# Kernel optimization log

Hardware: AMD Instinct MI355X
Metric: run time of the kernel (lower is better)

Reference implementation:

```python
import jax, jax.numpy as jnp
import numpy as np

N_NODES = 50000
N_EDGES = 600000
N_GRAPHS = 256
BN_EPS = 1e-5
NEG_SLOPE = 0.2  # PyG GATv2 default leaky_relu slope


def segment_softmax(logits, seg, num_segments):
    # logits: [E, H], softmax over edges sharing the same destination node
    m = jax.ops.segment_max(logits, seg, num_segments=num_segments)
    e = jnp.exp(logits - m[seg])
    s = jax.ops.segment_sum(e, seg, num_segments=num_segments)
    return e / (s[seg] + 1e-16)


def gatv2_layer(h, edge_attr, src, dst, Wl, bl, Wr, br, We, att, bias, concat):
    # PyG GATv2Conv (share_weights=False, edge_dim set), eval mode (no dropout)
    heads, out_c = att.shape
    N = h.shape[0]
    xl = (h @ Wl + bl).reshape(N, heads, out_c)  # messages from source
    xr = (h @ Wr + br).reshape(N, heads, out_c)  # destination term
    em = (edge_attr @ We).reshape(-1, heads, out_c)
    z = jax.nn.leaky_relu(xl[src] + xr[dst] + em, NEG_SLOPE)  # [E,H,C]
    logits = jnp.einsum('ehc,hc->eh', z, att)
    alpha = segment_softmax(logits, dst, N)  # [E,H]
    out = jax.ops.segment_sum(xl[src] * alpha[:, :, None], dst, num_segments=N)
    out = out.reshape(N, heads * out_c) if concat else out.mean(axis=1)
    return out + bias


def batch_norm(h, gamma, beta):
    mu = h.mean(axis=0)
    var = h.var(axis=0)
    return gamma * (h - mu) * jax.lax.rsqrt(var + BN_EPS) + beta


def setup_inputs() -> dict:
    key = jax.random.key(0)
    ks = jax.random.split(key, 32)
    F, Fe, H, C = 64, 16, 4, 64
    HC = H * C

    def w(k, shape):
        return jax.random.normal(k, shape, dtype=jnp.float32) * 0.1

    inp = {
        'x': jax.random.normal(ks[0], (N_NODES, F), dtype=jnp.float32),
        'edge_attr': jax.random.normal(ks[1], (N_EDGES, Fe), dtype=jnp.float32),
        'edge_index': jax.random.randint(ks[2], (2, N_EDGES), 0, N_NODES, dtype=jnp.int32),
        'batch': jnp.sort(jax.random.randint(ks[3], (N_NODES,), 0, N_GRAPHS, dtype=jnp.int32)),
        # input projection
        'W_in': w(ks[4], (F, C)), 'b_in': jnp.zeros((C,), jnp.float32),
        'Wl0': w(ks[5], (C, HC)), 'bl0': jnp.zeros((HC,), jnp.float32),
        'Wr0': w(ks[6], (C, HC)), 'br0': jnp.zeros((HC,), jnp.float32),
        'We0': w(ks[7], (Fe, HC)),
        'att0': w(ks[8], (H, C)), 'bias0': jnp.zeros((HC,), jnp.float32),
        'g0': jnp.ones((HC,), jnp.float32), 'beta0': jnp.zeros((HC,), jnp.float32),
        'Wl1': w(ks[9], (HC, HC)), 'bl1': jnp.zeros((HC,), jnp.float32),
        'Wr1': w(ks[10], (HC, HC)), 'br1': jnp.zeros((HC,), jnp.float32),
        'We1': w(ks[11], (Fe, HC)),
        'att1': w(ks[12], (H, C)), 'bias1': jnp.zeros((C,), jnp.float32),
        'g1': jnp.ones((C,), jnp.float32), 'beta1': jnp.zeros((C,), jnp.float32),
        # MLP head 64 -> 32 -> 16 -> 1
        'Wm1': w(ks[13], (C, C // 2)), 'bm1': jnp.zeros((C // 2,), jnp.float32),
        'Wm2': w(ks[14], (C // 2, C // 4)), 'bm2': jnp.zeros((C // 4,), jnp.float32),
        'Wm3': w(ks[15], (C // 4, 1)), 'bm3': jnp.zeros((1,), jnp.float32),
    }
    return inp


def reference(x, edge_attr, W_in, b_in,
              Wl0, bl0, Wr0, br0, We0, att0, bias0, g0, beta0,
              Wl1, bl1, Wr1, br1, We1, att1, bias1, g1, beta1,
              Wm1, bm1, Wm2, bm2, Wm3, bm3,
              edge_index, batch):
    src, dst = edge_index[0], edge_index[1]
    h = jax.nn.relu(x @ W_in + b_in)
    h = gatv2_layer(h, edge_attr, src, dst, Wl0, bl0, Wr0, br0, We0, att0, bias0, True)
    h = batch_norm(h, g0, beta0)
    h = jax.nn.relu(h)  # dropout is identity in eval mode
    h = gatv2_layer(h, edge_attr, src, dst, Wl1, bl1, Wr1, br1, We1, att1, bias1, False)
    h = batch_norm(h, g1, beta1)
    # global mean pool over graphs
    cnt = jax.ops.segment_sum(jnp.ones((h.shape[0],), h.dtype), batch, num_segments=N_GRAPHS)
    pooled = jax.ops.segment_sum(h, batch, num_segments=N_GRAPHS) / jnp.maximum(cnt, 1.0)[:, None]
    z = jax.nn.relu(pooled @ Wm1 + bm1)
    z = jax.nn.relu(z @ Wm2 + bm2)
    return z @ Wm3 + bm3  # [N_GRAPHS, 1]
```

## Files before the change

### kernel.cpp

```cpp
#include <hip/hip_runtime.h>
#include <math.h>

constexpr int NN = 50000;
constexpr int NE = 600000;
constexpr int NG = 256;
constexpr int SB = (NN + 255) / 256;
constexpr float kBnEps = 1e-5f;
constexpr float kSlope = 0.2f;

typedef _Float16 f16x8 __attribute__((ext_vector_type(8)));
typedef float f32x16 __attribute__((ext_vector_type(16)));

__device__ __forceinline__ float rdlane(float v, int l) {
    return __builtin_bit_cast(float, __builtin_amdgcn_readlane(__builtin_bit_cast(int, v), l));
}

template <int CTRL>
__device__ __forceinline__ float dppadd(float v) {
    int t = __builtin_amdgcn_mov_dpp(__builtin_bit_cast(int, v), CTRL, 0xF, 0xF, true);
    return v + __builtin_bit_cast(float, t);
}
__device__ __forceinline__ float sum16(float v) {
    v = dppadd<0xB1>(v);
    v = dppadd<0x4E>(v);
    v = dppadd<0x141>(v);
    v = dppadd<0x140>(v);
    return v;
}

__device__ __forceinline__ float4 fma4(float a, float4 b, float4 c) {
    c.x = fmaf(a, b.x, c.x); c.y = fmaf(a, b.y, c.y);
    c.z = fmaf(a, b.z, c.z); c.w = fmaf(a, b.w, c.w);
    return c;
}

__global__ __launch_bounds__(256) void k_hist(const int* __restrict__ dst, int* __restrict__ cnt)
{
    int e = blockIdx.x * 256 + threadIdx.x;
    if (e < NE) atomicAdd(&cnt[dst[e]], 1);
}

__global__ __launch_bounds__(256) void k_scanA(const int* __restrict__ cnt,
                                               int* __restrict__ offs, int* __restrict__ bsum)
{
    __shared__ int s[256];
    int tid = threadIdx.x;
    int i = blockIdx.x * 256 + tid;
    int v = (i < NN) ? cnt[i] : 0;
    s[tid] = v;
    __syncthreads();
    #pragma unroll
    for (int d = 1; d < 256; d <<= 1) {
        int u = (tid >= d) ? s[tid - d] : 0;
        __syncthreads();
        s[tid] += u;
        __syncthreads();
    }
    if (i < NN) offs[i] = s[tid];
    if (tid == 255) bsum[blockIdx.x] = s[255];
}

__global__ __launch_bounds__(256) void k_scanC(const int* __restrict__ cnt,
                                               const int* __restrict__ bsum,
                                               int* __restrict__ offs, int* __restrict__ cur)
{
    __shared__ int sred[256];
    int t = threadIdx.x;
    int b = blockIdx.x;
    int v = (t < SB && t < b) ? bsum[t] : 0;
    sred[t] = v;
    __syncthreads();
    #pragma unroll
    for (int d = 128; d > 0; d >>= 1) {
        if (t < d) sred[t] += sred[t + d];
        __syncthreads();
    }
    int pre = sred[0];
    int i = b * 256 + t;
    if (i > NN) return;
    if (i == NN) { offs[NN] = NE; return; }
    int w = offs[i] - cnt[i] + pre;
    offs[i] = w;
    cur[i] = w;
}

__global__ __launch_bounds__(256) void k_scatter_light(const int* __restrict__ dst,
                                                       const int* __restrict__ src,
                                                       int* __restrict__ cur,
                                                       int2* __restrict__ se)
{
    int e = blockIdx.x * 256 + threadIdx.x;
    if (e < NE) {
        int p = atomicAdd(&cur[dst[e]], 1);
        se[p] = make_int2(src[e], e);
    }
}

__device__ __forceinline__ void prep_w_body(int T, const float* __restrict__ WL,
                                            const float* __restrict__ WR,
                                            _Float16* __restrict__ bhi,
                                            _Float16* __restrict__ blo)
{
    int g   = T & 1;
    int col = (T >> 1) & 511;
    int kt  = T >> 10;
    const float* W = (col < 256) ? WL : WR;
    int c = col & 255;
    f16x8 h8, l8;
    #pragma unroll
    for (int i = 0; i < 8; ++i) {
        float v = W[(size_t)(kt * 16 + g * 8 + i) * 256 + c];
        _Float16 hv = (_Float16)v;
        h8[i] = hv;
        l8[i] = (_Float16)(v - (float)hv);
    }
    *(f16x8*)(bhi + (size_t)T * 8) = h8;
    *(f16x8*)(blo + (size_t)T * 8) = l8;
}

__global__ __launch_bounds__(256) void k_prep_all(
    const float* __restrict__ Wl0, const float* __restrict__ Wr0,
    _Float16* __restrict__ bhi0, _Float16* __restrict__ blo0,
    const float* __restrict__ Wl1, const float* __restrict__ Wr1,
    _Float16* __restrict__ bhi1, _Float16* __restrict__ blo1)
{
    if (blockIdx.x < 16) {
        int T = blockIdx.x * 256 + threadIdx.x;
        prep_w_body(T, Wl0, Wr0, bhi0, blo0);
    } else {
        int T = (blockIdx.x - 16) * 256 + threadIdx.x;
        prep_w_body(T, Wl1, Wr1, bhi1, blo1);
    }
}

__global__ __launch_bounds__(512) void k_lin0_mfma(
    const float* __restrict__ x, const float* __restrict__ Win,
    const float* __restrict__ bin,
    const _Float16* __restrict__ Bhi, const _Float16* __restrict__ Blo,
    const float* __restrict__ bl, const float* __restrict__ br,
    float* __restrict__ outl, float* __restrict__ outr)
{
    __shared__ float h0s[64][68];
    __shared__ f16x8 Apack[2][4][128];
    int tid = threadIdx.x;
    int lane = tid & 63, wave = tid >> 6;
    int row0 = blockIdx.x * 64;

    {
        int rbase = row0 + wave * 8;
        float xreg[8];
        #pragma unroll
        for (int j = 0; j < 8; ++j) {
            int row = rbase + j; if (row >= NN) row = NN - 1;
            xreg[j] = x[(size_t)row * 64 + lane];
        }
        float b0 = bin[lane];
        float h0r[8];
        #pragma unroll
        for (int j = 0; j < 8; ++j) h0r[j] = b0;
        for (int k = 0; k < 64; ++k) {
            float w = Win[k * 64 + lane];
            #pragma unroll
            for (int j = 0; j < 8; ++j) h0r[j] = fmaf(rdlane(xreg[j], k), w, h0r[j]);
        }
        #pragma unroll
        for (int j = 0; j < 8; ++j)
            h0s[wave * 8 + j][lane] = fmaxf(h0r[j], 0.f);
    }
    __syncthreads();

    {
        int row = tid >> 3;
        int o = (tid & 7) * 8;
        f16x8 hi8, lo8;
        #pragma unroll
        for (int i = 0; i < 8; ++i) {
            float v = h0s[row][o + i];
            _Float16 hv = (_Float16)v;
            hi8[i] = hv;
            lo8[i] = (_Float16)(v - (float)hv);
        }
        int kt = o >> 4, g2 = (o >> 3) & 1;
        int slot = (g2 * 64 + row) ^ kt;
        Apack[0][kt][slot] = hi8;
        Apack[1][kt][slot] = lo8;
    }
    __syncthreads();

    int g = lane >> 5;
    int rowtile = wave >> 2;
    int colbase = (wave & 3) * 128 + (lane & 31);
    int aslot = g * 64 + rowtile * 32 + (lane & 31);
    f32x16 acc[4];
    #pragma unroll
    for (int nt = 0; nt < 4; ++nt)
        #pragma unroll
        for (int r = 0; r < 16; ++r) acc[nt][r] = 0.f;

    const f16x8* bh = (const f16x8*)Bhi;
    const f16x8* bo = (const f16x8*)Blo;
    size_t fbase = (size_t)colbase * 2 + g;

    #pragma unroll 1
    for (int kt = 0; kt < 4; ++kt) {
        f16x8 ahi = Apack[0][kt][aslot ^ kt];
        f16x8 alo = Apack[1][kt][aslot ^ kt];
        f16x8 wh[4], wl[4];
        #pragma unroll
        for (int nt = 0; nt < 4; ++nt) {
            size_t fi = fbase + (size_t)kt * 1024 + nt * 64;
            wh[nt] = bh[fi];
            wl[nt] = bo[fi];
        }
        #pragma unroll
        for (int nt = 0; nt < 4; ++nt)
            acc[nt] = __builtin_amdgcn_mfma_f32_32x32x16_f16(ahi, wh[nt], acc[nt], 0, 0, 0);
        #pragma unroll
        for (int nt = 0; nt < 4; ++nt)
            acc[nt] = __builtin_amdgcn_mfma_f32_32x32x16_f16(alo, wh[nt], acc[nt], 0, 0, 0);
        #pragma unroll
        for (int nt = 0; nt < 4; ++nt)
            acc[nt] = __builtin_amdgcn_mfma_f32_32x32x16_f16(ahi, wl[nt], acc[nt], 0, 0, 0);
    }

    #pragma unroll
    for (int nt = 0; nt < 4; ++nt) {
        int col = colbase + nt * 32;
        bool isR = col >= 256;
        int c = isR ? col - 256 : col;
        float bv = isR ? br[c] : bl[c];
        float* outp = isR ? outr : outl;
        #pragma unroll
        for (int r = 0; r < 16; ++r) {
            int rowoff = (r & 3) + 8 * (r >> 2) + 4 * g;
            int grow = row0 + rowtile * 32 + rowoff;
            if (grow < NN)
                outp[(size_t)grow * 256 + c] = acc[nt][r] + bv;
        }
    }
}

__global__ __launch_bounds__(512) void k_linear2_mfma(
    const float* __restrict__ h, const _Float16* __restrict__ Bhi,
    const _Float16* __restrict__ Blo, const float* __restrict__ bl,
    const float* __restrict__ br, const float* __restrict__ scale,
    const float* __restrict__ shift, float* __restrict__ outl,
    float* __restrict__ outr)
{
    __shared__ f16x8 Apack[2][16][128];
    int tid = threadIdx.x;
    int lane = tid & 63, wave = tid >> 6;
    int row0 = blockIdx.x * 64;

    {
        int row  = tid >> 3;
        int koff = (tid & 7) * 32;
        int grow = row0 + row; if (grow >= NN) grow = NN - 1;
        const float* hp = h + (size_t)grow * 256 + koff;
        #pragma unroll
        for (int j2 = 0; j2 < 4; ++j2) {
            int o = koff + j2 * 8;
            float4 a  = *(const float4*)(hp + j2 * 8);
            float4 b  = *(const float4*)(hp + j2 * 8 + 4);
            float4 s0 = *(const float4*)(scale + o);
            float4 s1 = *(const float4*)(scale + o + 4);
            float4 f0 = *(const float4*)(shift + o);
            float4 f1 = *(const float4*)(shift + o + 4);
            float va[8] = {
                fmaxf(fmaf(a.x, s0.x, f0.x), 0.f), fmaxf(fmaf(a.y, s0.y, f0.y), 0.f),
                fmaxf(fmaf(a.z, s0.z, f0.z), 0.f), fmaxf(fmaf(a.w, s0.w, f0.w), 0.f),
                fmaxf(fmaf(b.x, s1.x, f1.x), 0.f), fmaxf(fmaf(b.y, s1.y, f1.y), 0.f),
                fmaxf(fmaf(b.z, s1.z, f1.z), 0.f), fmaxf(fmaf(b.w, s1.w, f1.w), 0.f)};
            f16x8 hi8, lo8;
            #pragma unroll
            for (int i = 0; i < 8; ++i) {
                _Float16 hv = (_Float16)va[i];
                hi8[i] = hv;
                lo8[i] = (_Float16)(va[i] - (float)hv);
            }
            int kt = o >> 4, g = (o >> 3) & 1;
            int slot = (g * 64 + row) ^ (kt & 7);
            Apack[0][kt][slot] = hi8;
            Apack[1][kt][slot] = lo8;
        }
    }
    __syncthreads();

    int g = lane >> 5;
    int rowtile = wave >> 2;
    int colbase = (wave & 3) * 128 + (lane & 31);
    int aslot = g * 64 + rowtile * 32 + (lane & 31);
    f32x16 acc[4];
    #pragma unroll
    for (int nt = 0; nt < 4; ++nt)
        #pragma unroll
        for (int r = 0; r < 16; ++r) acc[nt][r] = 0.f;

    const f16x8* bh = (const f16x8*)Bhi;
    const f16x8* bo = (const f16x8*)Blo;
    size_t fbase = (size_t)colbase * 2 + g;

    #pragma unroll 1
    for (int kt = 0; kt < 16; ++kt) {
        f16x8 ahi = Apack[0][kt][aslot ^ (kt & 7)];
        f16x8 alo = Apack[1][kt][aslot ^ (kt & 7)];
        f16x8 wh[4], wl[4];
        #pragma unroll
        for (int nt = 0; nt < 4; ++nt) {
            size_t fi = fbase + (size_t)kt * 1024 + nt * 64;
            wh[nt] = bh[fi];
            wl[nt] = bo[fi];
        }
        #pragma unroll
        for (int nt = 0; nt < 4; ++nt)
            acc[nt] = __builtin_amdgcn_mfma_f32_32x32x16_f16(ahi, wh[nt], acc[nt], 0, 0, 0);
        #pragma unroll
        for (int nt = 0; nt < 4; ++nt)
            acc[nt] = __builtin_amdgcn_mfma_f32_32x32x16_f16(alo, wh[nt], acc[nt], 0, 0, 0);
        #pragma unroll
        for (int nt = 0; nt < 4; ++nt)
            acc[nt] = __builtin_amdgcn_mfma_f32_32x32x16_f16(ahi, wl[nt], acc[nt], 0, 0, 0);
    }

    #pragma unroll
    for (int nt = 0; nt < 4; ++nt) {
        int col = colbase + nt * 32;
        bool isR = col >= 256;
        int c = isR ? col - 256 : col;
        float bv = isR ? br[c] : bl[c];
        float* outp = isR ? outr : outl;
        #pragma unroll
        for (int r = 0; r < 16; ++r) {
            int rowoff = (r & 3) + 8 * (r >> 2) + 4 * g;
            int grow = row0 + rowtile * 32 + rowoff;
            if (grow < NN)
                outp[(size_t)grow * 256 + c] = acc[nt][r] + bv;
        }
    }
}

template <bool CONCAT, int NPW>
__global__ __launch_bounds__(256) void k_attn(
    const float* __restrict__ xl, const float* __restrict__ xr,
    const int2* __restrict__ se, const float* __restrict__ ea,
    const float* __restrict__ We, const float* __restrict__ att,
    const int* __restrict__ offs, const float* __restrict__ bias,
    float* __restrict__ out)
{
    int tid = threadIdx.x;
    int lane = tid & 63, wave = tid >> 6;
    float4 wr[16];
    #pragma unroll
    for (int k = 0; k < 16; ++k) wr[k] = ((const float4*)(We + k * 256))[lane];
    float4 ar = ((const float4*)att)[lane];

    int g16 = lane >> 4;
    int k16 = lane & 15;
    int nodebase = (blockIdx.x * 4 + wave) * NPW;
    if (nodebase >= NN) return;

    for (int nn = 0; nn < NPW; ++nn) {
        int n = nodebase + nn;
        if (n >= NN) break;
        int beg = offs[n], end = offs[n + 1];
        float4 xr4 = ((const float4*)(xr + (size_t)n * 256))[lane];

        float m = -INFINITY, ssum = 0.f;
        float4 acc = make_float4(0.f, 0.f, 0.f, 0.f);

        float nea = 0.f;
        float4 nx0, nx1, nx2, nx3;

        auto loadbatch = [&](int i) {
            int idx = i + g16;
            if (idx > end - 1) idx = end - 1;
            int2 sv2 = se[idx];
            nea = ea[(size_t)sv2.y * 16 + k16];
            int sv = sv2.x;
            int s0 = __builtin_amdgcn_readlane(sv, 0);
            int s1 = __builtin_amdgcn_readlane(sv, 16);
            int s2 = __builtin_amdgcn_readlane(sv, 32);
            int s3 = __builtin_amdgcn_readlane(sv, 48);
            nx0 = ((const float4*)(xl + (size_t)s0 * 256))[lane];
            nx1 = ((const float4*)(xl + (size_t)s1 * 256))[lane];
            nx2 = ((const float4*)(xl + (size_t)s2 * 256))[lane];
            nx3 = ((const float4*)(xl + (size_t)s3 * 256))[lane];
        };

        if (beg < end) loadbatch(beg);

        for (int i = beg; i < end; i += 4) {
            float cea = nea;
            float4 x0 = nx0, x1 = nx1, x2 = nx2, x3 = nx3;
            if (i + 4 < end) loadbatch(i + 4);

            float p[4];
            #pragma unroll
            for (int g = 0; g < 4; ++g) {
                float4 xg = (g == 0) ? x0 : (g == 1) ? x1 : (g == 2) ? x2 : x3;
                float4 em = xr4;
                #pragma unroll
                for (int k = 0; k < 16; ++k) {
                    float a = rdlane(cea, g * 16 + k);
                    em.x = fmaf(a, wr[k].x, em.x);
                    em.y = fmaf(a, wr[k].y, em.y);
                    em.z = fmaf(a, wr[k].z, em.z);
                    em.w = fmaf(a, wr[k].w, em.w);
                }
                float z0 = xg.x + em.x;
                float z1 = xg.y + em.y;
                float z2 = xg.z + em.z;
                float z3 = xg.w + em.w;
                z0 = (z0 > 0.f) ? z0 : kSlope * z0;
                z1 = (z1 > 0.f) ? z1 : kSlope * z1;
                z2 = (z2 > 0.f) ? z2 : kSlope * z2;
                z3 = (z3 > 0.f) ? z3 : kSlope * z3;
                float pv = fmaf(z0, ar.x, fmaf(z1, ar.y, fmaf(z2, ar.z, z3 * ar.w)));
                pv = sum16(pv);
                p[g] = (i + g < end) ? pv : -INFINITY;
            }
            float pm = fmaxf(fmaxf(p[0], p[1]), fmaxf(p[2], p[3]));
            float mn = fmaxf(m, pm);
            float sc = __expf(m - mn);
            float w0 = __expf(p[0] - mn);
            float w1 = __expf(p[1] - mn);
            float w2 = __expf(p[2] - mn);
            float w3 = __expf(p[3] - mn);
            ssum = fmaf(ssum, sc, (w0 + w1) + (w2 + w3));
            acc.x = fmaf(acc.x, sc, fmaf(w0, x0.x, fmaf(w1, x1.x, fmaf(w2, x2.x, w3 * x3.x))));
            acc.y = fmaf(acc.y, sc, fmaf(w0, x0.y, fmaf(w1, x1.y, fmaf(w2, x2.y, w3 * x3.y))));
            acc.z = fmaf(acc.z, sc, fmaf(w0, x0.z, fmaf(w1, x1.z, fmaf(w2, x2.z, w3 * x3.z))));
            acc.w = fmaf(acc.w, sc, fmaf(w0, x0.w, fmaf(w1, x1.w, fmaf(w2, x2.w, w3 * x3.w))));
            m = mn;
        }

        float inv = 1.f / (ssum + 1e-16f);
        if (CONCAT) {
            float4 b4 = ((const float4*)bias)[lane];
            float4 o;
            o.x = fmaf(acc.x, inv, b4.x);
            o.y = fmaf(acc.y, inv, b4.y);
            o.z = fmaf(acc.z, inv, b4.z);
            o.w = fmaf(acc.w, inv, b4.w);
            ((float4*)(out + (size_t)n * 256))[lane] = o;
        } else {
            float v0 = acc.x * inv, v1 = acc.y * inv, v2 = acc.z * inv, v3 = acc.w * inv;
            v0 += __shfl_xor(v0, 16, 64); v0 += __shfl_xor(v0, 32, 64);
            v1 += __shfl_xor(v1, 16, 64); v1 += __shfl_xor(v1, 32, 64);
            v2 += __shfl_xor(v2, 16, 64); v2 += __shfl_xor(v2, 32, 64);
            v3 += __shfl_xor(v3, 16, 64); v3 += __shfl_xor(v3, 32, 64);
            if (lane < 16) {
                float4 b4 = ((const float4*)bias)[lane];
                float4 o;
                o.x = fmaf(0.25f, v0, b4.x);
                o.y = fmaf(0.25f, v1, b4.y);
                o.z = fmaf(0.25f, v2, b4.z);
                o.w = fmaf(0.25f, v3, b4.w);
                ((float4*)(out + (size_t)n * 64))[lane] = o;
            }
        }
    }
}

template <int CH>
__global__ __launch_bounds__(256) void k_bn_stats(const float* __restrict__ h,
                                                  float* __restrict__ sum,
                                                  float* __restrict__ sumsq)
{
    constexpr int RP = 256 / CH;
    int tid = threadIdx.x;
    int c = tid % CH;
    int rsub = tid / CH;
    float s = 0.f, q = 0.f;
    #pragma unroll 4
    for (int n = blockIdx.x * RP + rsub; n < NN; n += gridDim.x * RP) {
        float v = h[(size_t)n * CH + c];
        s += v; q = fmaf(v, v, q);
    }
    __shared__ float ls[256], lq[256];
    ls[tid] = s; lq[tid] = q;
    __syncthreads();
    if (tid < CH) {
        #pragma unroll
        for (int r = 1; r < RP; ++r) { s += ls[tid + r * CH]; q += lq[tid + r * CH]; }
        atomicAdd(&sum[tid], s);
        atomicAdd(&sumsq[tid], q);
    }
}

__global__ void k_bn_finalize(const float* __restrict__ sum, const float* __restrict__ sumsq,
                              const float* __restrict__ g, const float* __restrict__ beta,
                              float* __restrict__ scale, float* __restrict__ shift, int CH)
{
    int c = threadIdx.x;
    if (c >= CH) return;
    float inv_n = 1.f / (float)NN;
    float mu = sum[c] * inv_n;
    float var = sumsq[c] * inv_n - mu * mu;
    float sc = g[c] / sqrtf(var + kBnEps);
    scale[c] = sc;
    shift[c] = fmaf(-mu, sc, beta[c]);
}

__global__ __launch_bounds__(256) void k_pool_mlp(
    const float* __restrict__ h2, const float* __restrict__ bns,
    const float* __restrict__ bnq, const float* __restrict__ gam,
    const float* __restrict__ beta, const int* __restrict__ batch,
    const float* __restrict__ Wm1, const float* __restrict__ bm1,
    const float* __restrict__ Wm2, const float* __restrict__ bm2,
    const float* __restrict__ Wm3, const float* __restrict__ bm3,
    float* __restrict__ out)
{
    int g = blockIdx.x, tid = threadIdx.x;
    int lane = tid & 63, wave = tid >> 6;
    __shared__ int sb[2];
    if (tid < 2) {
        int target = g + tid;
        int lo = 0, hi = NN;
        while (lo < hi) {
            int mid = (lo + hi) >> 1;
            if (batch[mid] < target) lo = mid + 1; else hi = mid;
        }
        sb[tid] = lo;
    }
    __syncthreads();
    int s = sb[0], e = sb[1];
    float inv_n = 1.f / (float)NN;
    float mu = bns[lane] * inv_n;
    float var = bnq[lane] * inv_n - mu * mu;
    float sc = gam[lane] / sqrtf(var + kBnEps);
    float sh = fmaf(-mu, sc, beta[lane]);
    float acc = 0.f;
    #pragma unroll 4
    for (int n = s + wave; n < e; n += 4)
        acc += fmaf(h2[(size_t)n * 64 + lane], sc, sh);
    __shared__ float red[4][64];
    red[wave][lane] = acc;
    __syncthreads();
    __shared__ float p[64], z1[32], z2[16];
    if (tid < 64) {
        float cnt = (float)(e - s);
        float a = red[0][tid] + red[1][tid] + red[2][tid] + red[3][tid];
        p[tid] = a / fmaxf(cnt, 1.f);
    }
    __syncthreads();
    if (tid < 32) {
        float a = bm1[tid];
        #pragma unroll
        for (int k = 0; k < 64; ++k) a = fmaf(p[k], Wm1[k * 32 + tid], a);
        z1[tid] = fmaxf(a, 0.f);
    }
    __syncthreads();
    if (tid < 16) {
        float a = bm2[tid];
        #pragma unroll
        for (int k = 0; k < 32; ++k) a = fmaf(z1[k], Wm2[k * 16 + tid], a);
        z2[tid] = fmaxf(a, 0.f);
    }
    __syncthreads();
    if (tid == 0) {
        float a = bm3[0];
        #pragma unroll
        for (int k = 0; k < 16; ++k) a = fmaf(z2[k], Wm3[k], a);
        out[g] = a;
    }
}

extern "C" void kernel_launch(void* const* d_in, const int* in_sizes, int n_in,
                              void* d_out, int out_size, void* d_ws, size_t ws_size,
                              hipStream_t stream)
{
    const float* x     = (const float*)d_in[0];
    const float* ea    = (const float*)d_in[1];
    const int*   ei    = (const int*)d_in[2];
    const int*   bat   = (const int*)d_in[3];
    const float* W_in  = (const float*)d_in[4];
    const float* b_in  = (const float*)d_in[5];
    const float* Wl0   = (const float*)d_in[6];
    const float* bl0   = (const float*)d_in[7];
    const float* Wr0   = (const float*)d_in[8];
    const float* br0   = (const float*)d_in[9];
    const float* We0   = (const float*)d_in[10];
    const float* att0  = (const float*)d_in[11];
    const float* bias0 = (const float*)d_in[12];
    const float* g0    = (const float*)d_in[13];
    const float* beta0 = (const float*)d_in[14];
    const float* Wl1   = (const float*)d_in[15];
    const float* bl1   = (const float*)d_in[16];
    const float* Wr1   = (const float*)d_in[17];
    const float* br1   = (const float*)d_in[18];
    const float* We1   = (const float*)d_in[19];
    const float* att1  = (const float*)d_in[20];
    const float* bias1 = (const float*)d_in[21];
    const float* g1    = (const float*)d_in[22];
    const float* beta1 = (const float*)d_in[23];
    const float* Wm1   = (const float*)d_in[24];
    const float* bm1   = (const float*)d_in[25];
    const float* Wm2   = (const float*)d_in[26];
    const float* bm2   = (const float*)d_in[27];
    const float* Wm3   = (const float*)d_in[28];
    const float* bm3   = (const float*)d_in[29];
    const int* src = ei;
    const int* dst = ei + NE;
    float* out = (float*)d_out;

    char* p = (char*)d_ws;
    auto take = [&](size_t nbytes) -> char* {
        char* q = p;
        p += (nbytes + 255) & ~(size_t)255;
        return q;
    };
    char* z0 = p;
    int*   hist   = (int*)take((size_t)NN * 4);
    float* bns0   = (float*)take(256 * 4);
    float* bnq0   = (float*)take(256 * 4);
    float* bns1   = (float*)take(64 * 4);
    float* bnq1   = (float*)take(64 * 4);
    size_t zbytes = (size_t)(p - z0);
    int*   offs   = (int*)take((size_t)(NN + 1) * 4);
    int*   curs   = (int*)take((size_t)NN * 4);
    int*   bsum   = (int*)take((size_t)SB * 4);
    int2*  se     = (int2*)take((size_t)NE * 8);
    float* h2     = (float*)take((size_t)NN * 64 * 4);
    float* xl     = (float*)take((size_t)NN * 256 * 4);
    float* xr     = (float*)take((size_t)NN * 256 * 4);
    float* h1     = (float*)take((size_t)NN * 256 * 4);
    float* scale0 = (float*)take(256 * 4);
    float* shift0 = (float*)take(256 * 4);
    _Float16* Bhi1 = (_Float16*)take((size_t)256 * 512 * 2);
    _Float16* Blo1 = (_Float16*)take((size_t)256 * 512 * 2);
    _Float16* Bhi0 = (_Float16*)take((size_t)64 * 512 * 2);
    _Float16* Blo0 = (_Float16*)take((size_t)64 * 512 * 2);

    hipMemsetAsync(z0, 0, zbytes, stream);

    k_hist<<<(NE + 255) / 256, 256, 0, stream>>>(dst, hist);
    k_prep_all<<<80, 256, 0, stream>>>(Wl0, Wr0, Bhi0, Blo0, Wl1, Wr1, Bhi1, Blo1);
    k_scanA<<<SB, 256, 0, stream>>>(hist, offs, bsum);
    k_scanC<<<SB, 256, 0, stream>>>(hist, bsum, offs, curs);
    k_scatter_light<<<(NE + 255) / 256, 256, 0, stream>>>(dst, src, curs, se);

    constexpr int NPW = 2;
    int attn_blocks = (NN + 4 * NPW - 1) / (4 * NPW);
    int lin_blocks = (NN + 63) / 64;

    k_lin0_mfma<<<lin_blocks, 512, 0, stream>>>(
        x, W_in, b_in, Bhi0, Blo0, bl0, br0, xl, xr);
    k_attn<true, NPW><<<attn_blocks, 256, 0, stream>>>(
        xl, xr, se, ea, We0, att0, offs, bias0, h1);
    k_bn_stats<256><<<256, 256, 0, stream>>>(h1, bns0, bnq0);
    k_bn_finalize<<<1, 256, 0, stream>>>(bns0, bnq0, g0, beta0, scale0, shift0, 256);

    k_linear2_mfma<<<lin_blocks, 512, 0, stream>>>(
        h1, Bhi1, Blo1, bl1, br1, scale0, shift0, xl, xr);
    k_attn<false, NPW><<<attn_blocks, 256, 0, stream>>>(
        xl, xr, se, ea, We1, att1, offs, bias1, h2);
    k_bn_stats<64><<<256, 256, 0, stream>>>(h2, bns1, bnq1);

    k_pool_mlp<<<NG, 256, 0, stream>>>(h2, bns1, bnq1, g1, beta1, bat,
                                       Wm1, bm1, Wm2, bm2, Wm3, bm3, out);
}
```

Before: 706.2 us.

## Make layer-1 linear persistent with weights held in registers

The layer-1 linear kernel becomes persistent with a fixed grid of 512 blocks. Each block owns one 128-column quarter of the output, and each wave keeps its 32-column slice of the split-f16 weights in registers for the whole kernel. Blocks loop over 32-row tiles, staging BN+ReLU-transformed activations into LDS, so weights are no longer reloaded from global memory for every 64-row tile. In exchange, each activation row is now read by four blocks and every tile needs two barriers. The BN-stats kernels are also launched with four times as many blocks.

```diff
diff --git a/kernel.cpp b/kernel.cpp
--- a/kernel.cpp
+++ b/kernel.cpp
@@ -240,101 +240,93 @@
     }
 }
 
-__global__ __launch_bounds__(512) void k_linear2_mfma(
+__global__ __launch_bounds__(256) void k_linear2_mfma(
     const float* __restrict__ h, const _Float16* __restrict__ Bhi,
     const _Float16* __restrict__ Blo, const float* __restrict__ bl,
     const float* __restrict__ br, const float* __restrict__ scale,
     const float* __restrict__ shift, float* __restrict__ outl,
     float* __restrict__ outr)
 {
-    __shared__ f16x8 Apack[2][16][128];
+    __shared__ f16x8 Apack[2][16][64];
     int tid = threadIdx.x;
     int lane = tid & 63, wave = tid >> 6;
-    int row0 = blockIdx.x * 64;
-
-    {
-        int row  = tid >> 3;
-        int koff = (tid & 7) * 32;
-        int grow = row0 + row; if (grow >= NN) grow = NN - 1;
-        const float* hp = h + (size_t)grow * 256 + koff;
-        #pragma unroll
-        for (int j2 = 0; j2 < 4; ++j2) {
-            int o = koff + j2 * 8;
-            float4 a  = *(const float4*)(hp + j2 * 8);
-            float4 b  = *(const float4*)(hp + j2 * 8 + 4);
-            float4 s0 = *(const float4*)(scale + o);
-            float4 s1 = *(const float4*)(scale + o + 4);
-            float4 f0 = *(const float4*)(shift + o);
-            float4 f1 = *(const float4*)(shift + o + 4);
-            float va[8] = {
-                fmaxf(fmaf(a.x, s0.x, f0.x), 0.f), fmaxf(fmaf(a.y, s0.y, f0.y), 0.f),
-                fmaxf(fmaf(a.z, s0.z, f0.z), 0.f), fmaxf(fmaf(a.w, s0.w, f0.w), 0.f),
-                fmaxf(fmaf(b.x, s1.x, f1.x), 0.f), fmaxf(fmaf(b.y, s1.y, f1.y), 0.f),
-                fmaxf(fmaf(b.z, s1.z, f1.z), 0.f), fmaxf(fmaf(b.w, s1.w, f1.w), 0.f)};
-            f16x8 hi8, lo8;
-            #pragma unroll
-            for (int i = 0; i < 8; ++i) {
-                _Float16 hv = (_Float16)va[i];
-                hi8[i] = hv;
-                lo8[i] = (_Float16)(va[i] - (float)hv);
-            }
-            int kt = o >> 4, g = (o >> 3) & 1;
-            int slot = (g * 64 + row) ^ (kt & 7);
-            Apack[0][kt][slot] = hi8;
-            Apack[1][kt][slot] = lo8;
-        }
-    }
-    __syncthreads();
-
+    int q = blockIdx.x & 3;
+    int mslot = blockIdx.x >> 2;
     int g = lane >> 5;
-    int rowtile = wave >> 2;
-    int colbase = (wave & 3) * 128 + (lane & 31);
-    int aslot = g * 64 + rowtile * 32 + (lane & 31);
-    f32x16 acc[4];
-    #pragma unroll
-    for (int nt = 0; nt < 4; ++nt)
-        #pragma unroll
-        for (int r = 0; r < 16; ++r) acc[nt][r] = 0.f;
+    int colbase = q * 128 + wave * 32 + (lane & 31);
+    size_t fbase = (size_t)colbase * 2 + g;
 
     const f16x8* bh = (const f16x8*)Bhi;
     const f16x8* bo = (const f16x8*)Blo;
-    size_t fbase = (size_t)colbase * 2 + g;
-
-    #pragma unroll 1
+    f16x8 BH[16], BL[16];
+    #pragma unroll
     for (int kt = 0; kt < 16; ++kt) {
-        f16x8 ahi = Apack[0][kt][aslot ^ (kt & 7)];
-        f16x8 alo = Apack[1][kt][aslot ^ (kt & 7)];
-        f16x8 wh[4], wl[4];
-        #pragma unroll
-        for (int nt = 0; nt < 4; ++nt) {
-            size_t fi = fbase + (size_t)kt * 1024 + nt * 64;
-            wh[nt] = bh[fi];
-            wl[nt] = bo[fi];
-        }
-        #pragma unroll
-        for (int nt = 0; nt < 4; ++nt)
-            acc[nt] = __builtin_amdgcn_mfma_f32_32x32x16_f16(ahi, wh[nt], acc[nt], 0, 0, 0);
-        #pragma unroll
-        for (int nt = 0; nt < 4; ++nt)
-            acc[nt] = __builtin_amdgcn_mfma_f32_32x32x16_f16(alo, wh[nt], acc[nt], 0, 0, 0);
-        #pragma unroll
-        for (int nt = 0; nt < 4; ++nt)
-            acc[nt] = __builtin_amdgcn_mfma_f32_32x32x16_f16(ahi, wl[nt], acc[nt], 0, 0, 0);
-    }
-
-    #pragma unroll
-    for (int nt = 0; nt < 4; ++nt) {
-        int col = colbase + nt * 32;
-        bool isR = col >= 256;
-        int c = isR ? col - 256 : col;
-        float bv = isR ? br[c] : bl[c];
-        float* outp = isR ? outr : outl;
+        BH[kt] = bh[fbase + (size_t)kt * 1024];
+        BL[kt] = bo[fbase + (size_t)kt * 1024];
+    }
+
+    bool isR = colbase >= 256;
+    int c = isR ? colbase - 256 : colbase;
+    float bv = isR ? br[c] : bl[c];
+    float* outp = isR ? outr : outl;
+
+    constexpr int NT = (NN + 31) / 32;
+    for (int t = mslot; t < NT; t += 128) {
+        int row0 = t * 32;
+        {
+            int row  = tid >> 3;
+            int koff = (tid & 7) * 32;
+            int grow = row0 + row; if (grow >= NN) grow = NN - 1;
+            const float* hp = h + (size_t)grow * 256 + koff;
+            #pragma unroll
+            for (int j2 = 0; j2 < 4; ++j2) {
+                int o = koff + j2 * 8;
+                float4 a  = *(const float4*)(hp + j2 * 8);
+                float4 b  = *(const float4*)(hp + j2 * 8 + 4);
+                float4 s0 = *(const float4*)(scale + o);
+                float4 s1 = *(const float4*)(scale + o + 4);
+                float4 f0 = *(const float4*)(shift + o);
+                float4 f1 = *(const float4*)(shift + o + 4);
+                float va[8] = {
+                    fmaxf(fmaf(a.x, s0.x, f0.x), 0.f), fmaxf(fmaf(a.y, s0.y, f0.y), 0.f),
+                    fmaxf(fmaf(a.z, s0.z, f0.z), 0.f), fmaxf(fmaf(a.w, s0.w, f0.w), 0.f),
+                    fmaxf(fmaf(b.x, s1.x, f1.x), 0.f), fmaxf(fmaf(b.y, s1.y, f1.y), 0.f),
+                    fmaxf(fmaf(b.z, s1.z, f1.z), 0.f), fmaxf(fmaf(b.w, s1.w, f1.w), 0.f)};
+                f16x8 hi8, lo8;
+                #pragma unroll
+                for (int i = 0; i < 8; ++i) {
+                    _Float16 hv = (_Float16)va[i];
+                    hi8[i] = hv;
+                    lo8[i] = (_Float16)(va[i] - (float)hv);
+                }
+                int kt = o >> 4, g2 = (o >> 3) & 1;
+                int slot = (g2 * 32 + row) ^ (kt & 7);
+                Apack[0][kt][slot] = hi8;
+                Apack[1][kt][slot] = lo8;
+            }
+        }
+        __syncthreads();
+
+        f32x16 acc;
+        #pragma unroll
+        for (int r = 0; r < 16; ++r) acc[r] = 0.f;
+
+        #pragma unroll
+        for (int kt = 0; kt < 16; ++kt) {
+            f16x8 ahi = Apack[0][kt][lane ^ (kt & 7)];
+            f16x8 alo = Apack[1][kt][lane ^ (kt & 7)];
+            acc = __builtin_amdgcn_mfma_f32_32x32x16_f16(ahi, BH[kt], acc, 0, 0, 0);
+            acc = __builtin_amdgcn_mfma_f32_32x32x16_f16(alo, BH[kt], acc, 0, 0, 0);
+            acc = __builtin_amdgcn_mfma_f32_32x32x16_f16(ahi, BL[kt], acc, 0, 0, 0);
+        }
+        __syncthreads();
+
         #pragma unroll
         for (int r = 0; r < 16; ++r) {
             int rowoff = (r & 3) + 8 * (r >> 2) + 4 * g;
-            int grow = row0 + rowtile * 32 + rowoff;
+            int grow = row0 + rowoff;
             if (grow < NN)
-                outp[(size_t)grow * 256 + c] = acc[nt][r] + bv;
+                outp[(size_t)grow * 256 + c] = acc[r] + bv;
         }
     }
 }
@@ -642,20 +634,20 @@
 
     constexpr int NPW = 2;
     int attn_blocks = (NN + 4 * NPW - 1) / (4 * NPW);
-    int lin_blocks = (NN + 63) / 64;
-
-    k_lin0_mfma<<<lin_blocks, 512, 0, stream>>>(
+    int lin0_blocks = (NN + 63) / 64;
+
+    k_lin0_mfma<<<lin0_blocks, 512, 0, stream>>>(
         x, W_in, b_in, Bhi0, Blo0, bl0, br0, xl, xr);
     k_attn<true, NPW><<<attn_blocks, 256, 0, stream>>>(
         xl, xr, se, ea, We0, att0, offs, bias0, h1);
-    k_bn_stats<256><<<256, 256, 0, stream>>>(h1, bns0, bnq0);
+    k_bn_stats<256><<<1024, 256, 0, stream>>>(h1, bns0, bnq0);
     k_bn_finalize<<<1, 256, 0, stream>>>(bns0, bnq0, g0, beta0, scale0, shift0, 256);
 
-    k_linear2_mfma<<<lin_blocks, 512, 0, stream>>>(
+    k_linear2_mfma<<<512, 256, 0, stream>>>(
         h1, Bhi1, Blo1, bl1, br1, scale0, shift0, xl, xr);
     k_attn<false, NPW><<<attn_blocks, 256, 0, stream>>>(
         xl, xr, se, ea, We1, att1, offs, bias1, h2);
-    k_bn_stats<64><<<256, 256, 0, stream>>>(h2, bns1, bnq1);
+    k_bn_stats<64><<<1024, 256, 0, stream>>>(h2, bns1, bnq1);
 
     k_pool_mlp<<<NG, 256, 0, stream>>>(h2, bns1, bnq1, g1, beta1, bat,
                                        Wm1, bm1, Wm2, bm2, Wm3, bm3, out);
```

Measured after the change: 677.0 us. -4.1%, faster.
